# Kernel tuning notes

Hardware: AMD Instinct MI355X
Metric: run time of the kernel (lower is better)

The kernel has to match this reference:

```python
import jax, jax.numpy as jnp
import numpy as np

N_NODES = 50000


def setup_inputs() -> dict:
    key = jax.random.key(0)
    k1, k2, k3 = jax.random.split(key, 3)
    x = jax.random.normal(k1, (N_NODES, 128), dtype=jnp.float32)
    edge_index = jax.random.randint(k2, (2, 800000), 0, N_NODES, dtype=jnp.int32)
    W = jax.random.normal(k3, (128, 128), dtype=jnp.float32) * (1.0 / np.sqrt(128.0))
    b = jnp.zeros((128,), dtype=jnp.float32)
    return {"x": x, "edge_index": edge_index, "W": W, "b": b}


def reference(x, edge_index, W, b):
    # DGL GraphConv with norm='both': h = D_in^{-1/2} A D_out^{-1/2} x W + b, then ReLU.
    src, dst = edge_index[0], edge_index[1]
    n = x.shape[0]
    ones = jnp.ones(src.shape, dtype=x.dtype)
    deg_out = jax.ops.segment_sum(ones, src, num_segments=n)  # out-degree of source
    deg_in = jax.ops.segment_sum(ones, dst, num_segments=n)   # in-degree of destination
    norm_src = jax.lax.rsqrt(jnp.maximum(deg_out, 1.0))       # [N]
    norm_dst = jax.lax.rsqrt(jnp.maximum(deg_in, 1.0))        # [N]
    h = x * norm_src[:, None]                                 # [N, d]
    agg = jax.ops.segment_sum(h[src], dst, num_segments=n)    # gather + scatter-add
    agg = agg * norm_dst[:, None]
    out = jnp.maximum(agg @ W + b, 0.0)                       # linear + ReLU
    return out
```

## Files before the change

kernel.cpp:

```cpp
#include <hip/hip_runtime.h>

#define N_NODES 50000
#define N_EDGES 800000
#define DIM 128
#define NHB 64
#define EPB (N_EDGES / NHB)
#define NPACK (N_NODES / 2)
#define SCAN_ELEMS 1024
#define SCAN_BLOCKS ((N_NODES + SCAN_ELEMS - 1) / SCAN_ELEMS)

typedef unsigned int uint;

__device__ __forceinline__ uint bf16pair(float a, float b) {
  uint ua = __float_as_uint(a); ua = (ua + 0x7FFFu + ((ua >> 16) & 1u)) >> 16;
  uint ub = __float_as_uint(b); ub = (ub + 0x7FFFu + ((ub >> 16) & 1u)) >> 16;
  return ua | (ub << 16);
}

__global__ __launch_bounds__(1024) void hist_kernel(
    const int* __restrict__ src, const int* __restrict__ dst,
    uint* __restrict__ hist_src, uint* __restrict__ hist_dst) {
  extern __shared__ uint h[];
  int b = blockIdx.x, t = threadIdx.x;
  int e0 = b * EPB;

  for (int i = t; i < NPACK; i += 1024) h[i] = 0;
  __syncthreads();
  for (int i = t; i < EPB; i += 1024) {
    int d = dst[e0 + i];
    atomicAdd(&h[d >> 1], 1u << ((d & 1) << 4));
  }
  __syncthreads();
  for (int i = t; i < NPACK; i += 1024) hist_dst[b * NPACK + i] = h[i];
  __syncthreads();

  for (int i = t; i < NPACK; i += 1024) h[i] = 0;
  __syncthreads();
  for (int i = t; i < EPB; i += 1024) {
    int s = src[e0 + i];
    atomicAdd(&h[s >> 1], 1u << ((s & 1) << 4));
  }
  __syncthreads();
  for (int i = t; i < NPACK; i += 1024) hist_src[b * NPACK + i] = h[i];
}

__global__ __launch_bounds__(256) void prefix_kernel(
    const uint* __restrict__ hist_src, const uint* __restrict__ hist_dst,
    uint* __restrict__ Ppack, int* __restrict__ cnt_in,
    float* __restrict__ norm_in, float* __restrict__ norm_out) {
  int i = blockIdx.x * 256 + threadIdx.x;
  if (i >= NPACK) return;
  uint r0 = 0, r1 = 0;
#pragma unroll 4
  for (int b = 0; b < NHB; ++b) {
    uint v = hist_dst[b * NPACK + i];
    Ppack[b * NPACK + i] = (r0 & 0xFFFFu) | (r1 << 16);
    r0 += v & 0xFFFFu; r1 += v >> 16;
  }
  cnt_in[2 * i] = (int)r0; cnt_in[2 * i + 1] = (int)r1;
  norm_in[2 * i]     = rsqrtf(fmaxf((float)r0, 1.0f));
  norm_in[2 * i + 1] = rsqrtf(fmaxf((float)r1, 1.0f));
  uint s0 = 0, s1 = 0;
#pragma unroll 4
  for (int b = 0; b < NHB; ++b) {
    uint v = hist_src[b * NPACK + i];
    s0 += v & 0xFFFFu; s1 += v >> 16;
  }
  norm_out[2 * i]     = rsqrtf(fmaxf((float)s0, 1.0f));
  norm_out[2 * i + 1] = rsqrtf(fmaxf((float)s1, 1.0f));
}

__global__ __launch_bounds__(256) void scan1_kernel(
    const int* __restrict__ counts, int* __restrict__ partial,
    int* __restrict__ blockSums, int n) {
  __shared__ int wsum[4];
  int t = threadIdx.x;
  int base = blockIdx.x * SCAN_ELEMS + t * 4;
  int c[4];
#pragma unroll
  for (int i = 0; i < 4; ++i) c[i] = (base + i < n) ? counts[base + i] : 0;
  int s = c[0] + c[1] + c[2] + c[3];
  int lane = t & 63, wid = t >> 6;
  int v = s;
#pragma unroll
  for (int off = 1; off < 64; off <<= 1) {
    int u = __shfl_up(v, off);
    if (lane >= off) v += u;
  }
  if (lane == 63) wsum[wid] = v;
  __syncthreads();
  if (t == 0) {
    int run = 0;
#pragma unroll
    for (int i = 0; i < 4; ++i) { int tmp = wsum[i]; wsum[i] = run; run += tmp; }
    blockSums[blockIdx.x] = run;
  }
  __syncthreads();
  int excl = wsum[wid] + v - s;
  int o0 = excl;
  int o1 = o0 + c[0];
  int o2 = o1 + c[1];
  int o3 = o2 + c[2];
  if (base + 0 < n) partial[base + 0] = o0;
  if (base + 1 < n) partial[base + 1] = o1;
  if (base + 2 < n) partial[base + 2] = o2;
  if (base + 3 < n) partial[base + 3] = o3;
}

__global__ void scan2_kernel(int* __restrict__ blockSums, int nb) {
  if (threadIdx.x == 0 && blockIdx.x == 0) {
    int run = 0;
    for (int i = 0; i < nb; ++i) { int t = blockSums[i]; blockSums[i] = run; run += t; }
  }
}

__global__ __launch_bounds__(256) void scan3_kernel(
    const int* __restrict__ partial, const int* __restrict__ blockSums,
    int* __restrict__ offsets, int n, int E) {
  int t = threadIdx.x;
  int bo = blockSums[blockIdx.x];
  int base = blockIdx.x * SCAN_ELEMS + t * 4;
#pragma unroll
  for (int i = 0; i < 4; ++i) {
    int idx = base + i;
    if (idx < n) offsets[idx] = partial[idx] + bo;
  }
  if (blockIdx.x == 0 && t == 0) offsets[n] = E;
}

__global__ __launch_bounds__(1024) void fill_kernel(
    const int* __restrict__ src, const int* __restrict__ dst,
    const int* __restrict__ offsets, const uint* __restrict__ Ppack,
    int* __restrict__ csr_src) {
  extern __shared__ uint cur[];
  int b = blockIdx.x, t = threadIdx.x;
  for (int i = t; i < NPACK; i += 1024) cur[i] = 0;
  __syncthreads();
  int e0 = b * EPB;
  const uint* Pb = Ppack + b * NPACK;
  for (int i = t; i < EPB; i += 1024) {
    int d = dst[e0 + i];
    int s = src[e0 + i];
    uint sh = (uint)(d & 1) << 4;
    uint old = atomicAdd(&cur[d >> 1], 1u << sh);
    uint lpos = (old >> sh) & 0xFFFFu;
    uint pbase = (Pb[d >> 1] >> sh) & 0xFFFFu;
    csr_src[offsets[d] + (int)pbase + (int)lpos] = s;
  }
}

__global__ __launch_bounds__(256) void gemm_kernel(
    const float4* __restrict__ x4, const float4* __restrict__ W4,
    const float* __restrict__ norm_out, uint2* __restrict__ yb2, int n) {
  __shared__ float4 Wl4[DIM * 32];
  int t = threadIdx.x;
#pragma unroll
  for (int i = 0; i < 16; ++i) Wl4[t + 256 * i] = W4[t + 256 * i];
  __syncthreads();

  int col4 = t & 31;
  int rg = t >> 5;
  int row0 = blockIdx.x * 64 + rg * 8;

  float4 acc[8];
#pragma unroll
  for (int i = 0; i < 8; ++i) acc[i] = make_float4(0.f, 0.f, 0.f, 0.f);

#pragma unroll 2
  for (int kc = 0; kc < 32; ++kc) {
    float4 w0 = Wl4[(4 * kc + 0) * 32 + col4];
    float4 w1 = Wl4[(4 * kc + 1) * 32 + col4];
    float4 w2 = Wl4[(4 * kc + 2) * 32 + col4];
    float4 w3 = Wl4[(4 * kc + 3) * 32 + col4];
#pragma unroll
    for (int i = 0; i < 8; ++i) {
      int gr = row0 + i;
      int cr = gr < n ? gr : n - 1;
      float4 a = x4[(size_t)cr * 32 + kc];
      acc[i].x = fmaf(a.x, w0.x, fmaf(a.y, w1.x, fmaf(a.z, w2.x, fmaf(a.w, w3.x, acc[i].x))));
      acc[i].y = fmaf(a.x, w0.y, fmaf(a.y, w1.y, fmaf(a.z, w2.y, fmaf(a.w, w3.y, acc[i].y))));
      acc[i].z = fmaf(a.x, w0.z, fmaf(a.y, w1.z, fmaf(a.z, w2.z, fmaf(a.w, w3.z, acc[i].z))));
      acc[i].w = fmaf(a.x, w0.w, fmaf(a.y, w1.w, fmaf(a.z, w2.w, fmaf(a.w, w3.w, acc[i].w))));
    }
  }

#pragma unroll
  for (int i = 0; i < 8; ++i) {
    int gr = row0 + i;
    if (gr < n) {
      float ns = norm_out[gr];
      float4 o = acc[i];
      uint2 packed;
      packed.x = bf16pair(o.x * ns, o.y * ns);
      packed.y = bf16pair(o.z * ns, o.w * ns);
      yb2[(size_t)gr * 32 + col4] = packed;
    }
  }
}

__global__ __launch_bounds__(256) void aggregate_kernel(
    const uint* __restrict__ yb, const int* __restrict__ csr_src,
    const int* __restrict__ offsets, const float* __restrict__ norm_in,
    const float2* __restrict__ b2, float2* __restrict__ out2, int n) {
  int t = threadIdx.x;
  int node = blockIdx.x * 4 + (t >> 6);
  if (node >= n) return;
  int lane = t & 63;
  int beg = offsets[node], end = offsets[node + 1];

  float ax0 = 0.f, ay0 = 0.f, ax1 = 0.f, ay1 = 0.f;
  float ax2 = 0.f, ay2 = 0.f, ax3 = 0.f, ay3 = 0.f;
  int j = beg;
  for (; j + 4 <= end; j += 4) {
    int s0 = csr_src[j + 0];
    int s1 = csr_src[j + 1];
    int s2 = csr_src[j + 2];
    int s3 = csr_src[j + 3];
    uint u0 = yb[(size_t)s0 * 64 + lane];
    uint u1 = yb[(size_t)s1 * 64 + lane];
    uint u2 = yb[(size_t)s2 * 64 + lane];
    uint u3 = yb[(size_t)s3 * 64 + lane];
    ax0 += __uint_as_float(u0 << 16);
    ay0 += __uint_as_float(u0 & 0xFFFF0000u);
    ax1 += __uint_as_float(u1 << 16);
    ay1 += __uint_as_float(u1 & 0xFFFF0000u);
    ax2 += __uint_as_float(u2 << 16);
    ay2 += __uint_as_float(u2 & 0xFFFF0000u);
    ax3 += __uint_as_float(u3 << 16);
    ay3 += __uint_as_float(u3 & 0xFFFF0000u);
  }
  for (; j < end; ++j) {
    int s0 = csr_src[j];
    uint u0 = yb[(size_t)s0 * 64 + lane];
    ax0 += __uint_as_float(u0 << 16);
    ay0 += __uint_as_float(u0 & 0xFFFF0000u);
  }
  float sx = (ax0 + ax1) + (ax2 + ax3);
  float sy = (ay0 + ay1) + (ay2 + ay3);

  float ni = norm_in[node];
  float2 bb = b2[lane];
  float2 o;
  o.x = fmaxf(fmaf(sx, ni, bb.x), 0.f);
  o.y = fmaxf(fmaf(sy, ni, bb.y), 0.f);
  out2[(size_t)node * 64 + lane] = o;
}

extern "C" void kernel_launch(void* const* d_in, const int* in_sizes, int n_in,
                              void* d_out, int out_size, void* d_ws, size_t ws_size,
                              hipStream_t stream) {
  const float* x  = (const float*)d_in[0];
  const int* ei   = (const int*)d_in[1];
  const float* W  = (const float*)d_in[2];
  const float* b  = (const float*)d_in[3];
  float* out      = (float*)d_out;

  const int* src = ei;
  const int* dst = ei + N_EDGES;

  char* p = (char*)d_ws;
  uint* yb       = (uint*)p;   p += (size_t)N_NODES * DIM * sizeof(unsigned short);
  uint* hist_dst = (uint*)p;   p += (size_t)NHB * NPACK * sizeof(uint);
  uint* hist_src = (uint*)p;   p += (size_t)NHB * NPACK * sizeof(uint);
  uint* Ppack    = (uint*)p;   p += (size_t)NHB * NPACK * sizeof(uint);
  int* cnt_in    = (int*)p;    p += (size_t)N_NODES * sizeof(int);
  float* norm_in = (float*)p;  p += (size_t)N_NODES * sizeof(float);
  float* norm_out= (float*)p;  p += (size_t)N_NODES * sizeof(float);
  int* offsets   = (int*)p;    p += (size_t)(N_NODES + 1) * sizeof(int);
  int* partial   = (int*)p;    p += (size_t)N_NODES * sizeof(int);
  int* blockSums = (int*)p;    p += 64 * sizeof(int);
  int* csr_src   = (int*)hist_src;

  const size_t lds_bytes = (size_t)NPACK * sizeof(uint);

  hist_kernel<<<NHB, 1024, lds_bytes, stream>>>(src, dst, hist_src, hist_dst);
  prefix_kernel<<<(NPACK + 255) / 256, 256, 0, stream>>>(
      hist_src, hist_dst, Ppack, cnt_in, norm_in, norm_out);
  gemm_kernel<<<(N_NODES + 63) / 64, 256, 0, stream>>>(
      (const float4*)x, (const float4*)W, norm_out, (uint2*)yb, N_NODES);
  scan1_kernel<<<SCAN_BLOCKS, 256, 0, stream>>>(cnt_in, partial, blockSums, N_NODES);
  scan2_kernel<<<1, 64, 0, stream>>>(blockSums, SCAN_BLOCKS);
  scan3_kernel<<<SCAN_BLOCKS, 256, 0, stream>>>(partial, blockSums, offsets, N_NODES, N_EDGES);
  fill_kernel<<<NHB, 1024, lds_bytes, stream>>>(src, dst, offsets, Ppack, csr_src);
  aggregate_kernel<<<(N_NODES + 3) / 4, 256, 0, stream>>>(
      yb, csr_src, offsets, norm_in, (const float2*)b, (float2*)out, N_NODES);
}
```

Baseline: 228.7 us.

## Use bf16 MFMA for the dense transform with pre-transposed bf16 weights

Replaces the FP32 FMA GEMM, which staged W in shared memory, with a bf16 MFMA 16x16x32 path. A new small kernel converts W to a transposed bf16 copy in the workspace. Each wave keeps its weight fragments in registers and converts x rows to bf16 on the fly. This cuts ALU cost of the dense transform but rounds x and W to bf16 before multiplying, which lowers accuracy, and it writes the output as scattered 2-byte stores.

```diff
diff --git a/kernel.cpp b/kernel.cpp
--- a/kernel.cpp
+++ b/kernel.cpp
@@ -10,11 +10,19 @@
 #define SCAN_BLOCKS ((N_NODES + SCAN_ELEMS - 1) / SCAN_ELEMS)
 
 typedef unsigned int uint;
+typedef unsigned short ushort;
+typedef __attribute__((ext_vector_type(8))) short short8;
+typedef __attribute__((ext_vector_type(4))) float f32x4;
 
 __device__ __forceinline__ uint bf16pair(float a, float b) {
   uint ua = __float_as_uint(a); ua = (ua + 0x7FFFu + ((ua >> 16) & 1u)) >> 16;
   uint ub = __float_as_uint(b); ub = (ub + 0x7FFFu + ((ub >> 16) & 1u)) >> 16;
   return ua | (ub << 16);
+}
+
+__device__ __forceinline__ ushort bf16one(float a) {
+  uint u = __float_as_uint(a); u = (u + 0x7FFFu + ((u >> 16) & 1u)) >> 16;
+  return (ushort)u;
 }
 
 __global__ __launch_bounds__(1024) void hist_kernel(
@@ -149,51 +157,67 @@
   }
 }
 
+__global__ __launch_bounds__(256) void wcvt_kernel(
+    const float* __restrict__ W, ushort* __restrict__ wt) {
+  int i = blockIdx.x * 256 + threadIdx.x;
+  int c = i >> 7, k = i & 127;
+  wt[i] = bf16one(W[k * 128 + c]);
+}
+
 __global__ __launch_bounds__(256) void gemm_kernel(
-    const float4* __restrict__ x4, const float4* __restrict__ W4,
-    const float* __restrict__ norm_out, uint2* __restrict__ yb2, int n) {
-  __shared__ float4 Wl4[DIM * 32];
+    const float* __restrict__ x, const uint* __restrict__ wt,
+    const float* __restrict__ norm_out, ushort* __restrict__ yb, int n) {
   int t = threadIdx.x;
-#pragma unroll
-  for (int i = 0; i < 16; ++i) Wl4[t + 256 * i] = W4[t + 256 * i];
-  __syncthreads();
-
-  int col4 = t & 31;
-  int rg = t >> 5;
-  int row0 = blockIdx.x * 64 + rg * 8;
-
-  float4 acc[8];
-#pragma unroll
-  for (int i = 0; i < 8; ++i) acc[i] = make_float4(0.f, 0.f, 0.f, 0.f);
-
-#pragma unroll 2
-  for (int kc = 0; kc < 32; ++kc) {
-    float4 w0 = Wl4[(4 * kc + 0) * 32 + col4];
-    float4 w1 = Wl4[(4 * kc + 1) * 32 + col4];
-    float4 w2 = Wl4[(4 * kc + 2) * 32 + col4];
-    float4 w3 = Wl4[(4 * kc + 3) * 32 + col4];
-#pragma unroll
-    for (int i = 0; i < 8; ++i) {
-      int gr = row0 + i;
-      int cr = gr < n ? gr : n - 1;
-      float4 a = x4[(size_t)cr * 32 + kc];
-      acc[i].x = fmaf(a.x, w0.x, fmaf(a.y, w1.x, fmaf(a.z, w2.x, fmaf(a.w, w3.x, acc[i].x))));
-      acc[i].y = fmaf(a.x, w0.y, fmaf(a.y, w1.y, fmaf(a.z, w2.y, fmaf(a.w, w3.y, acc[i].y))));
-      acc[i].z = fmaf(a.x, w0.z, fmaf(a.y, w1.z, fmaf(a.z, w2.z, fmaf(a.w, w3.z, acc[i].z))));
-      acc[i].w = fmaf(a.x, w0.w, fmaf(a.y, w1.w, fmaf(a.z, w2.w, fmaf(a.w, w3.w, acc[i].w))));
+  int wid = t >> 6, lane = t & 63;
+  int lr = lane & 15;
+  int lk = lane >> 4;
+  int col0 = wid * 32;
+  int brow = blockIdx.x * 64;
+
+  uint4 bu[2][4];
+#pragma unroll
+  for (int ct = 0; ct < 2; ++ct) {
+    const uint* bp = wt + (col0 + ct * 16 + lr) * 64 + lk * 4;
+#pragma unroll
+    for (int kc = 0; kc < 4; ++kc)
+      bu[ct][kc] = *(const uint4*)(bp + kc * 16);
+  }
+
+#pragma unroll
+  for (int rt = 0; rt < 4; ++rt) {
+    int arow = brow + rt * 16 + lr;
+    int crow = arow < n ? arow : n - 1;
+    const float* ap = x + (size_t)crow * 128 + lk * 8;
+
+    uint4 au[4];
+#pragma unroll
+    for (int kc = 0; kc < 4; ++kc) {
+      float4 a0 = *(const float4*)(ap + kc * 32);
+      float4 a1 = *(const float4*)(ap + kc * 32 + 4);
+      uint4 u;
+      u.x = bf16pair(a0.x, a0.y); u.y = bf16pair(a0.z, a0.w);
+      u.z = bf16pair(a1.x, a1.y); u.w = bf16pair(a1.z, a1.w);
+      au[kc] = u;
     }
-  }
-
-#pragma unroll
-  for (int i = 0; i < 8; ++i) {
-    int gr = row0 + i;
-    if (gr < n) {
-      float ns = norm_out[gr];
-      float4 o = acc[i];
-      uint2 packed;
-      packed.x = bf16pair(o.x * ns, o.y * ns);
-      packed.y = bf16pair(o.z * ns, o.w * ns);
-      yb2[(size_t)gr * 32 + col4] = packed;
+
+    f32x4 acc0 = {0.f, 0.f, 0.f, 0.f};
+    f32x4 acc1 = {0.f, 0.f, 0.f, 0.f};
+#pragma unroll
+    for (int kc = 0; kc < 4; ++kc) {
+      short8 a = *(short8*)&au[kc];
+      acc0 = __builtin_amdgcn_mfma_f32_16x16x32_bf16(a, *(short8*)&bu[0][kc], acc0, 0, 0, 0);
+      acc1 = __builtin_amdgcn_mfma_f32_16x16x32_bf16(a, *(short8*)&bu[1][kc], acc1, 0, 0, 0);
+    }
+
+#pragma unroll
+    for (int j = 0; j < 4; ++j) {
+      int grow = brow + rt * 16 + lk * 4 + j;
+      if (grow < n) {
+        float ns = norm_out[grow];
+        size_t base = (size_t)grow * 128;
+        yb[base + col0 + lr]      = bf16one(acc0[j] * ns);
+        yb[base + col0 + 16 + lr] = bf16one(acc1[j] * ns);
+      }
     }
   }
 }
@@ -259,7 +283,8 @@
   const int* dst = ei + N_EDGES;
 
   char* p = (char*)d_ws;
-  uint* yb       = (uint*)p;   p += (size_t)N_NODES * DIM * sizeof(unsigned short);
+  uint* yb       = (uint*)p;   p += (size_t)N_NODES * DIM * sizeof(ushort);
+  ushort* wt     = (ushort*)p; p += (size_t)DIM * DIM * sizeof(ushort);
   uint* hist_dst = (uint*)p;   p += (size_t)NHB * NPACK * sizeof(uint);
   uint* hist_src = (uint*)p;   p += (size_t)NHB * NPACK * sizeof(uint);
   uint* Ppack    = (uint*)p;   p += (size_t)NHB * NPACK * sizeof(uint);
@@ -273,11 +298,12 @@
 
   const size_t lds_bytes = (size_t)NPACK * sizeof(uint);
 
+  wcvt_kernel<<<(DIM * DIM) / 256, 256, 0, stream>>>(W, wt);
   hist_kernel<<<NHB, 1024, lds_bytes, stream>>>(src, dst, hist_src, hist_dst);
   prefix_kernel<<<(NPACK + 255) / 256, 256, 0, stream>>>(
       hist_src, hist_dst, Ppack, cnt_in, norm_in, norm_out);
   gemm_kernel<<<(N_NODES + 63) / 64, 256, 0, stream>>>(
-      (const float4*)x, (const float4*)W, norm_out, (uint2*)yb, N_NODES);
+      x, (const uint*)wt, norm_out, (ushort*)yb, N_NODES);
   scan1_kernel<<<SCAN_BLOCKS, 256, 0, stream>>>(cnt_in, partial, blockSums, N_NODES);
   scan2_kernel<<<1, 64, 0, stream>>>(blockSums, SCAN_BLOCKS);
   scan3_kernel<<<SCAN_BLOCKS, 256, 0, stream>>>(partial, blockSums, offsets, N_NODES, N_EDGES);
```

Result: faster. 212.3 us (-7.2%).
